# Kernel tuning notes

Hardware: AMD Instinct MI355X
Metric: run time of the kernel (lower is better)

The kernel has to match this reference:

```python
import jax, jax.numpy as jnp
import numpy as np

DIM1, DIM2, NUM_ANS = 1024, 1024, 1000
B, T = 64, 128


def setup_inputs() -> dict:
    key = jax.random.key(0)
    ks = jax.random.split(key, 12)
    H, D_IN = DIM1, DIM1 + DIM2
    s = 0.02
    return {
        "data1": jax.random.normal(ks[0], (B, T, DIM1), dtype=jnp.float32),
        "data2": jax.random.normal(ks[1], (B, T, DIM2), dtype=jnp.float32),
        # layer-1 LSTM (input D_IN -> hidden H), PyTorch gate order i,f,g,o
        "W_ih1": jax.random.normal(ks[2], (4 * H, D_IN), dtype=jnp.float32) * s,
        "W_hh1": jax.random.normal(ks[3], (4 * H, H), dtype=jnp.float32) * s,
        "b1": jax.random.normal(ks[4], (4 * H,), dtype=jnp.float32) * s,
        # layer-2 LSTM (H -> H)
        "W_ih2": jax.random.normal(ks[5], (4 * H, H), dtype=jnp.float32) * s,
        "W_hh2": jax.random.normal(ks[6], (4 * H, H), dtype=jnp.float32) * s,
        "b2": jax.random.normal(ks[7], (4 * H,), dtype=jnp.float32) * s,
        # predict MLP: dim1 -> dim1//4 -> num_ans
        "Wp1": jax.random.normal(ks[8], (DIM1, DIM1 // 4), dtype=jnp.float32) * s,
        "bp1": jnp.zeros((DIM1 // 4,), dtype=jnp.float32),
        "Wp2": jax.random.normal(ks[9], (DIM1 // 4, NUM_ANS), dtype=jnp.float32) * s,
        "bp2": jnp.zeros((NUM_ANS,), dtype=jnp.float32),
    }


def _lstm_cell(x, h, c, Wih, Whh, b):
    gates = x @ Wih.T + h @ Whh.T + b  # [B, 4H]
    i, f, g, o = jnp.split(gates, 4, axis=-1)
    c_new = jax.nn.sigmoid(f) * c + jax.nn.sigmoid(i) * jnp.tanh(g)
    h_new = jax.nn.sigmoid(o) * jnp.tanh(c_new)
    return h_new, c_new


def reference(data1, data2, W_ih1, W_hh1, b1, W_ih2, W_hh2, b2, Wp1, bp1, Wp2, bp2):
    joint = jnp.concatenate((data1, data2), axis=-1)  # [B, T, dim1+dim2]
    Bb = joint.shape[0]
    H = W_hh1.shape[1]
    z = jnp.zeros((Bb, H), dtype=joint.dtype)

    def step(carry, x_t):
        h1, c1, h2, c2 = carry
        h1, c1 = _lstm_cell(x_t, h1, c1, W_ih1, W_hh1, b1)
        h2, c2 = _lstm_cell(h1, h2, c2, W_ih2, W_hh2, b2)
        out_t = h2 + h1  # residual connection between layers
        return (h1, c1, h2, c2), out_t

    xs = jnp.swapaxes(joint, 0, 1)  # [T, B, D]
    _, outs = jax.lax.scan(step, (z, z, z, z), xs)
    lstm_out = jnp.swapaxes(outs, 0, 1)  # [B, T, H]

    hid = jax.nn.relu(lstm_out @ Wp1 + bp1)  # dropout is identity at inference
    logits = hid @ Wp2 + bp2  # [B, T, num_ans]
    return jax.nn.softmax(jnp.squeeze(logits), axis=-1)
```

## Files before the change

kernel.cpp:

```cpp
#include <hip/hip_runtime.h>
#include <math.h>

#define BB   64
#define TT   128
#define HH   1024
#define DIN  2048
#define G4   4096
#define MALL 8192
#define NANS 1000

typedef __attribute__((ext_vector_type(8))) short bf16x8;
typedef __attribute__((ext_vector_type(4))) float f32x4;
typedef __attribute__((ext_vector_type(4))) unsigned int u32x4;

__device__ __forceinline__ float sigmoidf_(float x) { return 1.0f / (1.0f + expf(-x)); }

__device__ __forceinline__ unsigned short f2bf(float f) {
  unsigned u = __float_as_uint(f);
  u = (u + 0x7fff + ((u >> 16) & 1)) >> 16;
  return (unsigned short)u;
}
__device__ __forceinline__ float bf2f(unsigned short h) {
  return __uint_as_float(((unsigned)h) << 16);
}
__device__ __forceinline__ f32x4 mfma16(bf16x8 a, bf16x8 b, f32x4 c) {
  return __builtin_amdgcn_mfma_f32_16x16x32_bf16(a, b, c, 0, 0, 0);
}

__device__ __forceinline__ void stg_b128_sys(unsigned short* p, u32x4 v) {
  asm volatile("global_store_dwordx4 %0, %1, off sc0 sc1" :: "v"(p), "v"(v) : "memory");
}

__global__ __launch_bounds__(256) void concat_cast(
    const float* __restrict__ a, const float* __restrict__ b,
    unsigned short* __restrict__ o, int rshift, long total)
{
  long idx = ((long)blockIdx.x * 256 + threadIdx.x) * 4;
  if (idx >= total) return;
  int row = (int)(idx >> rshift);
  int col = (int)(idx & ((1L << rshift) - 1));
  int half = 1 << (rshift - 1);
  const float* s = (col < half) ? (a + (size_t)row * half + col)
                                : (b + (size_t)row * half + col - half);
  float4 v = *(const float4*)s;
  ushort4 ov;
  ov.x = f2bf(v.x); ov.y = f2bf(v.y); ov.z = f2bf(v.z); ov.w = f2bf(v.w);
  *(ushort4*)(o + idx) = ov;
}

__global__ __launch_bounds__(256) void cast_bf16(
    const float* __restrict__ s, unsigned short* __restrict__ o, long n)
{
  long idx = ((long)blockIdx.x * 256 + threadIdx.x) * 4;
  if (idx >= n) return;
  float4 v = *(const float4*)(s + idx);
  ushort4 ov;
  ov.x = f2bf(v.x); ov.y = f2bf(v.y); ov.z = f2bf(v.z); ov.w = f2bf(v.w);
  *(ushort4*)(o + idx) = ov;
}

__global__ __launch_bounds__(256) void cvt_wp1(
    const float* __restrict__ Wp1, unsigned short* __restrict__ o)
{
  int idx = blockIdx.x * 256 + threadIdx.x;
  int n = idx >> 10, k = idx & 1023;
  o[idx] = f2bf(Wp1[(size_t)k * 256 + n]);
}

__global__ __launch_bounds__(256) void cvt_wp2(
    const float* __restrict__ Wp2, unsigned short* __restrict__ o)
{
  int idx = blockIdx.x * 256 + threadIdx.x;
  int n = idx >> 8, k = idx & 255;
  o[idx] = f2bf(n < NANS ? Wp2[(size_t)k * NANS + n] : 0.f);
}

__global__ __launch_bounds__(256) void zero_ring(
    float4* __restrict__ a, float4* __restrict__ b, unsigned int* __restrict__ bar)
{
  int i = blockIdx.x * 256 + threadIdx.x;
  if (i < 8192) a[i] = make_float4(0.f, 0.f, 0.f, 0.f);
  else          b[i - 8192] = make_float4(0.f, 0.f, 0.f, 0.f);
  if (i == 0) *bar = 0u;
}

template<int OUT_BF16, int RELU, int PERM>
__global__ __launch_bounds__(256) void mfma_gemm(
    const unsigned short* __restrict__ A,
    const unsigned short* __restrict__ W,
    const float* __restrict__ bias,
    void* __restrict__ Cout,
    int M, int N, int K, int ldc, int nvalid)
{
  __shared__ __align__(16) unsigned short As[128 * 72];
  __shared__ __align__(16) unsigned short Bs[128 * 72];
  const int t = threadIdx.x;
  const int n0 = blockIdx.x * 128, m0 = blockIdx.y * 128;
  const int w = t >> 6, lane = t & 63, lr = lane & 15, q = lane >> 4;
  const int wn = (w & 1) * 64, wm = (w >> 1) * 64;
  f32x4 acc[4][4] = {};
  for (int k0 = 0; k0 < K; k0 += 64) {
    #pragma unroll
    for (int s = 0; s < 4; s++) {
      int ci = s * 256 + t;
      int row = ci >> 3, c = ci & 7;
      bf16x8 va = *(const bf16x8*)(A + (size_t)(m0 + row) * K + k0 + c * 8);
      *(bf16x8*)(As + row * 72 + c * 8) = va;
      bf16x8 vb = *(const bf16x8*)(W + (size_t)(n0 + row) * K + k0 + c * 8);
      *(bf16x8*)(Bs + row * 72 + c * 8) = vb;
    }
    __syncthreads();
    #pragma unroll
    for (int kk = 0; kk < 2; kk++) {
      bf16x8 a[4], b[4];
      #pragma unroll
      for (int mt = 0; mt < 4; mt++)
        a[mt] = *(const bf16x8*)(As + (wm + mt * 16 + lr) * 72 + kk * 32 + q * 8);
      #pragma unroll
      for (int nt = 0; nt < 4; nt++)
        b[nt] = *(const bf16x8*)(Bs + (wn + nt * 16 + lr) * 72 + kk * 32 + q * 8);
      #pragma unroll
      for (int mt = 0; mt < 4; mt++)
        #pragma unroll
        for (int nt = 0; nt < 4; nt++)
          acc[mt][nt] = mfma16(a[mt], b[nt], acc[mt][nt]);
    }
    __syncthreads();
  }
  #pragma unroll
  for (int mt = 0; mt < 4; mt++)
    #pragma unroll
    for (int nt = 0; nt < 4; nt++)
      #pragma unroll
      for (int r = 0; r < 4; r++) {
        int row = m0 + wm + mt * 16 + q * 4 + r;
        int col = n0 + wn + nt * 16 + lr;
        if (col < nvalid) {
          float v = acc[mt][nt][r] + bias[col];
          if (RELU) v = fmaxf(v, 0.f);
          if (PERM) row = ((row & 127) << 6) | (row >> 7);
          if (OUT_BF16)
            ((unsigned short*)Cout)[(size_t)row * ldc + col] = f2bf(v);
          else
            ((float*)Cout)[(size_t)row * ldc + col] = v;
        }
      }
}

__global__ __launch_bounds__(512) void lstm_persist(
    const unsigned short* __restrict__ Whh1b,
    const unsigned short* __restrict__ W2cat,
    const unsigned short* __restrict__ gxb,
    const float* __restrict__ b2,
    unsigned short* __restrict__ hr1,
    unsigned short* __restrict__ hr2,
    unsigned short* __restrict__ lob,
    unsigned int* __restrict__ bar)
{
  __shared__ float red[4][64][34];
  __shared__ __align__(16) unsigned short hst[64][8];
  const int t = threadIdx.x;
  const int w = t >> 6, lane = t & 63, lr = lane & 15, q = lane >> 4;
  const int kq = w & 3, rh = w >> 2;
  const bool isA = (blockIdx.x < 128);
  const int j0 = (isA ? blockIdx.x : blockIdx.x - 128) * 8;
  const int g0 = lr >> 2, u0 = lr & 3;
  const int cm = t >> 3, cu = t & 7, ju = j0 + cu;
  const int cb = (cu >> 2) * 17 + (cu & 3);
  float creg = 0.f;

  const unsigned short* wpA0 =
      Whh1b + (size_t)(g0 * 1024 + j0 + u0) * 1024 + kq * 256 + q * 8;
  const unsigned short* wpA1 = wpA0 + 4 * 1024;
  const unsigned short* wpB0 =
      W2cat + (size_t)(g0 * 1024 + j0 + u0) * 2048 + kq * 512 + q * 8;
  const unsigned short* wpB1 = wpB0 + 4 * 2048;

  for (int p = 0; p <= TT; p++) {
    if (isA) {
      if (p < TT) {
        const unsigned short* h1p = hr1 + (size_t)p * 65536;
        const unsigned short* gp = gxb + ((size_t)(p << 6) + cm) * 4096 + ju;
        unsigned short gi = gp[0], gf = gp[1024], gg2 = gp[2048], go = gp[3072];
        {
          const int kof = kq * 256 + q * 8;
          const unsigned short* hb = h1p + (size_t)(rh * 32 + lr) * 1024 + kof;
          f32x4 acc[2][2] = {};
          #pragma unroll
          for (int ks = 0; ks < 8; ks++) {
            bf16x8 b0 = *(const bf16x8*)(wpA0 + ks * 32);
            bf16x8 b1 = *(const bf16x8*)(wpA1 + ks * 32);
            #pragma unroll
            for (int mt = 0; mt < 2; mt++) {
              bf16x8 af = *(const bf16x8*)(hb + (size_t)(mt * 16) * 1024 + ks * 32);
              acc[mt][0] = mfma16(af, b0, acc[mt][0]);
              acc[mt][1] = mfma16(af, b1, acc[mt][1]);
            }
          }
          #pragma unroll
          for (int mt = 0; mt < 2; mt++)
            #pragma unroll
            for (int r = 0; r < 4; r++) {
              red[kq][rh * 32 + mt * 16 + q * 4 + r][lr]      = acc[mt][0][r];
              red[kq][rh * 32 + mt * 16 + q * 4 + r][17 + lr] = acc[mt][1][r];
            }
        }
        __syncthreads();
        float s[4];
        #pragma unroll
        for (int gg = 0; gg < 4; gg++)
          s[gg] = red[0][cm][cb + gg * 4] + red[1][cm][cb + gg * 4]
                + red[2][cm][cb + gg * 4] + red[3][cm][cb + gg * 4];
        s[0] += bf2f(gi); s[1] += bf2f(gf); s[2] += bf2f(gg2); s[3] += bf2f(go);
        float i_ = sigmoidf_(s[0]), f_ = sigmoidf_(s[1]);
        float g_ = tanhf(s[2]), o_ = sigmoidf_(s[3]);
        float c = f_ * creg + i_ * g_;
        creg = c;
        hst[cm][cu] = f2bf(o_ * tanhf(c));
        __syncthreads();
        if (t < 64) {
          u32x4 v = *(const u32x4*)(&hst[t][0]);
          stg_b128_sys(hr1 + (size_t)(p + 1) * 65536 + t * 1024 + j0, v);
        }
        asm volatile("s_waitcnt vmcnt(0)" ::: "memory");
      }
    } else {
      if (p > 0) {
        const unsigned short* h1p = hr1 + (size_t)p * 65536;
        const unsigned short* h2p = hr2 + (size_t)(p - 1) * 65536;
        {
          const int kof = kq * 512 + q * 8;
          const unsigned short* hb = (kq < 2)
              ? (h1p + (size_t)(rh * 32 + lr) * 1024 + kof)
              : (h2p + (size_t)(rh * 32 + lr) * 1024 + (kof - 1024));
          f32x4 acc[2][2] = {};
          #pragma unroll
          for (int ks = 0; ks < 16; ks++) {
            bf16x8 b0 = *(const bf16x8*)(wpB0 + ks * 32);
            bf16x8 b1 = *(const bf16x8*)(wpB1 + ks * 32);
            #pragma unroll
            for (int mt = 0; mt < 2; mt++) {
              bf16x8 af = *(const bf16x8*)(hb + (size_t)(mt * 16) * 1024 + ks * 32);
              acc[mt][0] = mfma16(af, b0, acc[mt][0]);
              acc[mt][1] = mfma16(af, b1, acc[mt][1]);
            }
          }
          #pragma unroll
          for (int mt = 0; mt < 2; mt++)
            #pragma unroll
            for (int r = 0; r < 4; r++) {
              red[kq][rh * 32 + mt * 16 + q * 4 + r][lr]      = acc[mt][0][r];
              red[kq][rh * 32 + mt * 16 + q * 4 + r][17 + lr] = acc[mt][1][r];
            }
        }
        __syncthreads();
        float s[4];
        #pragma unroll
        for (int gg = 0; gg < 4; gg++)
          s[gg] = red[0][cm][cb + gg * 4] + red[1][cm][cb + gg * 4]
                + red[2][cm][cb + gg * 4] + red[3][cm][cb + gg * 4]
                + b2[gg * 1024 + ju];
        float i_ = sigmoidf_(s[0]), f_ = sigmoidf_(s[1]);
        float g_ = tanhf(s[2]), o_ = sigmoidf_(s[3]);
        float c = f_ * creg + i_ * g_;
        creg = c;
        float h2v = o_ * tanhf(c);
        hst[cm][cu] = f2bf(h2v);
        float h1v = bf2f(h1p[(size_t)cm * 1024 + ju]);
        lob[((size_t)(cm << 7) + (p - 1)) * 1024 + ju] = f2bf(h1v + h2v);
        __syncthreads();
        if (t < 64) {
          u32x4 v = *(const u32x4*)(&hst[t][0]);
          stg_b128_sys(hr2 + (size_t)p * 65536 + t * 1024 + j0, v);
        }
        asm volatile("s_waitcnt vmcnt(0)" ::: "memory");
      }
    }

    if (p < TT) {
      __syncthreads();
      if (t == 0) {
        __hip_atomic_fetch_add(bar, 1u, __ATOMIC_RELAXED, __HIP_MEMORY_SCOPE_AGENT);
        const unsigned tgt = 256u * (unsigned)(p + 1);
        unsigned iters = 0;
        while (__hip_atomic_load(bar, __ATOMIC_RELAXED, __HIP_MEMORY_SCOPE_AGENT) < tgt) {
          __builtin_amdgcn_s_sleep(1);
          if (++iters > 100000000u) break;
        }
      }
      __syncthreads();
    }
  }
}

__global__ __launch_bounds__(256) void softmax_k(float* __restrict__ out)
{
  __shared__ float smax[4];
  __shared__ float ssum[4];
  const int m = blockIdx.x;
  const int t = threadIdx.x;
  const int lane = t & 63, wid = t >> 6;
  const bool act = (t < 250);
  float x[4] = {0.f, 0.f, 0.f, 0.f};
  if (act) *(float4*)x = *(const float4*)(out + (size_t)m * NANS + t * 4);
  float v = act ? fmaxf(fmaxf(x[0], x[1]), fmaxf(x[2], x[3])) : -1e30f;
  #pragma unroll
  for (int o = 32; o > 0; o >>= 1) v = fmaxf(v, __shfl_down(v, o));
  if (lane == 0) smax[wid] = v;
  __syncthreads();
  const float mx = fmaxf(fmaxf(smax[0], smax[1]), fmaxf(smax[2], smax[3]));
  float e[4] = {0.f, 0.f, 0.f, 0.f};
  float s = 0.f;
  if (act) {
    e[0] = expf(x[0] - mx); e[1] = expf(x[1] - mx);
    e[2] = expf(x[2] - mx); e[3] = expf(x[3] - mx);
    s = (e[0] + e[1]) + (e[2] + e[3]);
  }
  #pragma unroll
  for (int o = 32; o > 0; o >>= 1) s += __shfl_down(s, o);
  if (lane == 0) ssum[wid] = s;
  __syncthreads();
  const float inv = 1.0f / (((ssum[0] + ssum[1]) + (ssum[2] + ssum[3])));
  if (act) {
    float4 o4 = make_float4(e[0] * inv, e[1] * inv, e[2] * inv, e[3] * inv);
    *(float4*)(out + (size_t)m * NANS + t * 4) = o4;
  }
}

extern "C" void kernel_launch(void* const* d_in, const int* in_sizes, int n_in,
                              void* d_out, int out_size, void* d_ws, size_t ws_size,
                              hipStream_t stream)
{
  const float* d1   = (const float*)d_in[0];
  const float* d2   = (const float*)d_in[1];
  const float* Wih1 = (const float*)d_in[2];
  const float* Whh1 = (const float*)d_in[3];
  const float* b1   = (const float*)d_in[4];
  const float* Wih2 = (const float*)d_in[5];
  const float* Whh2 = (const float*)d_in[6];
  const float* b2   = (const float*)d_in[7];
  const float* Wp1  = (const float*)d_in[8];
  const float* bp1  = (const float*)d_in[9];
  const float* Wp2  = (const float*)d_in[10];
  const float* bp2  = (const float*)d_in[11];
  float* out = (float*)d_out;

  unsigned char* p = (unsigned char*)d_ws;
  unsigned short* gxb   = (unsigned short*)p;  p += 67108864;
  unsigned short* jb    = (unsigned short*)p;  p += 33554432;
  unsigned short* Wb1   = (unsigned short*)p;  p += 16777216;
  unsigned short* W2cat = (unsigned short*)p;  p += 16777216;
  unsigned short* Whh1b = (unsigned short*)p;  p += 8388608;
  unsigned short* lob   = (unsigned short*)p;  p += 16777216;
  unsigned short* hidb  = (unsigned short*)p;  p += 4194304;
  unsigned short* Wp1t  = (unsigned short*)p;  p += 524288;
  unsigned short* Wp2t  = (unsigned short*)p;  p += 524288;
  unsigned int*   bar   = (unsigned int*)p;    p += 256;
  if (ws_size < (size_t)(p - (unsigned char*)d_ws)) return;

  unsigned short* hr1 = jb;
  unsigned short* hr2 = jb + (size_t)129 * 65536;

  concat_cast<<<16384, 256, 0, stream>>>(d1, d2, jb, 11, 16777216L);
  cast_bf16<<<8192, 256, 0, stream>>>(Wih1, Wb1, 8388608L);
  cast_bf16<<<4096, 256, 0, stream>>>(Whh1, Whh1b, 4194304L);
  concat_cast<<<8192, 256, 0, stream>>>(Wih2, Whh2, W2cat, 11, 8388608L);
  cvt_wp1<<<1024, 256, 0, stream>>>(Wp1, Wp1t);
  cvt_wp2<<<1024, 256, 0, stream>>>(Wp2, Wp2t);

  mfma_gemm<1, 0, 1><<<dim3(32, 64), 256, 0, stream>>>(
      jb, Wb1, b1, gxb, MALL, G4, DIN, G4, G4);

  zero_ring<<<64, 256, 0, stream>>>((float4*)hr1, (float4*)hr2, bar);

  lstm_persist<<<256, 512, 0, stream>>>(Whh1b, W2cat, gxb, b2, hr1, hr2, lob, bar);

  mfma_gemm<1, 1, 0><<<dim3(2, 64), 256, 0, stream>>>(
      lob, Wp1t, bp1, hidb, MALL, 256, 1024, 256, 256);
  mfma_gemm<0, 0, 0><<<dim3(8, 64), 256, 0, stream>>>(
      hidb, Wp2t, bp2, out, MALL, 1024, 256, NANS, NANS);
  softmax_k<<<MALL, 256, 0, stream>>>(out);
}
```

Before: 3.181 ms.

## Replace atomic grid barrier with flag-based master barrier and prefetch h via asm loads

Replaces the single atomic-counter grid barrier with per-block arrival flags on separate cache lines. Block 0 gathers all 256 flags and then writes per-block release flags. Each step now issues all hidden-state loads up front through inline-asm global loads into registers, followed by one vmcnt wait, before the MFMA loop. It also adds launch_bounds occupancy of 2. The aim is to cut atomic contention and load-latency serialization in the latency-bound recurrent loop, at the cost of more registers and an extra hop through block 0 for release.

```diff
diff --git a/kernel.cpp b/kernel.cpp
--- a/kernel.cpp
+++ b/kernel.cpp
@@ -30,6 +30,16 @@
 __device__ __forceinline__ void stg_b128_sys(unsigned short* p, u32x4 v) {
   asm volatile("global_store_dwordx4 %0, %1, off sc0 sc1" :: "v"(p), "v"(v) : "memory");
 }
+__device__ __forceinline__ void stg_u32_sys(unsigned int* p, unsigned v) {
+  asm volatile("global_store_dword %0, %1, off sc0 sc1" :: "v"(p), "v"(v) : "memory");
+}
+__device__ __forceinline__ void ldg_b128(bf16x8* d, const unsigned short* p) {
+  asm volatile("global_load_dwordx4 %0, %1, off" : "=v"(*d) : "v"(p));
+}
+#define VMEM_FENCE() do { \
+  asm volatile("s_waitcnt vmcnt(0)" ::: "memory"); \
+  __builtin_amdgcn_sched_barrier(0); \
+} while (0)
 
 __global__ __launch_bounds__(256) void concat_cast(
     const float* __restrict__ a, const float* __restrict__ b,
@@ -76,12 +86,13 @@
 }
 
 __global__ __launch_bounds__(256) void zero_ring(
-    float4* __restrict__ a, float4* __restrict__ b, unsigned int* __restrict__ bar)
+    float4* __restrict__ a, float4* __restrict__ b, float4* __restrict__ f)
 {
   int i = blockIdx.x * 256 + threadIdx.x;
-  if (i < 8192) a[i] = make_float4(0.f, 0.f, 0.f, 0.f);
-  else          b[i - 8192] = make_float4(0.f, 0.f, 0.f, 0.f);
-  if (i == 0) *bar = 0u;
+  float4 z = make_float4(0.f, 0.f, 0.f, 0.f);
+  if (i < 8192)       a[i] = z;
+  else if (i < 16384) b[i - 8192] = z;
+  else if (i < 18432) f[i - 16384] = z;
 }
 
 template<int OUT_BF16, int RELU, int PERM>
@@ -147,7 +158,7 @@
       }
 }
 
-__global__ __launch_bounds__(512) void lstm_persist(
+__global__ __launch_bounds__(512, 2) void lstm_persist(
     const unsigned short* __restrict__ Whh1b,
     const unsigned short* __restrict__ W2cat,
     const unsigned short* __restrict__ gxb,
@@ -155,7 +166,8 @@
     unsigned short* __restrict__ hr1,
     unsigned short* __restrict__ hr2,
     unsigned short* __restrict__ lob,
-    unsigned int* __restrict__ bar)
+    unsigned int* __restrict__ abar,
+    unsigned int* __restrict__ rbar)
 {
   __shared__ float red[4][64][34];
   __shared__ __align__(16) unsigned short hst[64][8];
@@ -182,20 +194,27 @@
         const unsigned short* h1p = hr1 + (size_t)p * 65536;
         const unsigned short* gp = gxb + ((size_t)(p << 6) + cm) * 4096 + ju;
         unsigned short gi = gp[0], gf = gp[1024], gg2 = gp[2048], go = gp[3072];
+        bf16x8 hreg[16];
         {
           const int kof = kq * 256 + q * 8;
           const unsigned short* hb = h1p + (size_t)(rh * 32 + lr) * 1024 + kof;
+          #pragma unroll
+          for (int ks = 0; ks < 8; ks++) {
+            ldg_b128(&hreg[2 * ks],     hb + ks * 32);
+            ldg_b128(&hreg[2 * ks + 1], hb + (size_t)16 * 1024 + ks * 32);
+          }
+        }
+        VMEM_FENCE();
+        {
           f32x4 acc[2][2] = {};
           #pragma unroll
           for (int ks = 0; ks < 8; ks++) {
             bf16x8 b0 = *(const bf16x8*)(wpA0 + ks * 32);
             bf16x8 b1 = *(const bf16x8*)(wpA1 + ks * 32);
-            #pragma unroll
-            for (int mt = 0; mt < 2; mt++) {
-              bf16x8 af = *(const bf16x8*)(hb + (size_t)(mt * 16) * 1024 + ks * 32);
-              acc[mt][0] = mfma16(af, b0, acc[mt][0]);
-              acc[mt][1] = mfma16(af, b1, acc[mt][1]);
-            }
+            acc[0][0] = mfma16(hreg[2 * ks],     b0, acc[0][0]);
+            acc[0][1] = mfma16(hreg[2 * ks],     b1, acc[0][1]);
+            acc[1][0] = mfma16(hreg[2 * ks + 1], b0, acc[1][0]);
+            acc[1][1] = mfma16(hreg[2 * ks + 1], b1, acc[1][1]);
           }
           #pragma unroll
           for (int mt = 0; mt < 2; mt++)
@@ -228,22 +247,29 @@
       if (p > 0) {
         const unsigned short* h1p = hr1 + (size_t)p * 65536;
         const unsigned short* h2p = hr2 + (size_t)(p - 1) * 65536;
+        bf16x8 hreg[32];
         {
           const int kof = kq * 512 + q * 8;
           const unsigned short* hb = (kq < 2)
               ? (h1p + (size_t)(rh * 32 + lr) * 1024 + kof)
               : (h2p + (size_t)(rh * 32 + lr) * 1024 + (kof - 1024));
+          #pragma unroll
+          for (int ks = 0; ks < 16; ks++) {
+            ldg_b128(&hreg[2 * ks],     hb + ks * 32);
+            ldg_b128(&hreg[2 * ks + 1], hb + (size_t)16 * 1024 + ks * 32);
+          }
+        }
+        VMEM_FENCE();
+        {
           f32x4 acc[2][2] = {};
           #pragma unroll
           for (int ks = 0; ks < 16; ks++) {
             bf16x8 b0 = *(const bf16x8*)(wpB0 + ks * 32);
             bf16x8 b1 = *(const bf16x8*)(wpB1 + ks * 32);
-            #pragma unroll
-            for (int mt = 0; mt < 2; mt++) {
-              bf16x8 af = *(const bf16x8*)(hb + (size_t)(mt * 16) * 1024 + ks * 32);
-              acc[mt][0] = mfma16(af, b0, acc[mt][0]);
-              acc[mt][1] = mfma16(af, b1, acc[mt][1]);
-            }
+            acc[0][0] = mfma16(hreg[2 * ks],     b0, acc[0][0]);
+            acc[0][1] = mfma16(hreg[2 * ks],     b1, acc[0][1]);
+            acc[1][0] = mfma16(hreg[2 * ks + 1], b0, acc[1][0]);
+            acc[1][1] = mfma16(hreg[2 * ks + 1], b1, acc[1][1]);
           }
           #pragma unroll
           for (int mt = 0; mt < 2; mt++)
@@ -279,12 +305,27 @@
 
     if (p < TT) {
       __syncthreads();
+      const unsigned tgt = (unsigned)(p + 1);
+      if (t == 0)
+        stg_u32_sys(abar + (size_t)blockIdx.x * 16, tgt);
+      if (blockIdx.x == 0) {
+        if (t < 256) {
+          const unsigned int* fp = abar + (size_t)t * 16;
+          unsigned iters = 0;
+          while (__hip_atomic_load(fp, __ATOMIC_RELAXED, __HIP_MEMORY_SCOPE_AGENT) < tgt) {
+            __builtin_amdgcn_s_sleep(2);
+            if (++iters > 100000000u) break;
+          }
+        }
+        __syncthreads();
+        if (t < 256)
+          stg_u32_sys(rbar + (size_t)t * 16, tgt);
+      }
       if (t == 0) {
-        __hip_atomic_fetch_add(bar, 1u, __ATOMIC_RELAXED, __HIP_MEMORY_SCOPE_AGENT);
-        const unsigned tgt = 256u * (unsigned)(p + 1);
+        const unsigned int* rp = rbar + (size_t)blockIdx.x * 16;
         unsigned iters = 0;
-        while (__hip_atomic_load(bar, __ATOMIC_RELAXED, __HIP_MEMORY_SCOPE_AGENT) < tgt) {
-          __builtin_amdgcn_s_sleep(1);
+        while (__hip_atomic_load(rp, __ATOMIC_RELAXED, __HIP_MEMORY_SCOPE_AGENT) < tgt) {
+          __builtin_amdgcn_s_sleep(2);
           if (++iters > 100000000u) break;
         }
       }
@@ -355,7 +396,8 @@
   unsigned short* hidb  = (unsigned short*)p;  p += 4194304;
   unsigned short* Wp1t  = (unsigned short*)p;  p += 524288;
   unsigned short* Wp2t  = (unsigned short*)p;  p += 524288;
-  unsigned int*   bar   = (unsigned int*)p;    p += 256;
+  unsigned int*   abar  = (unsigned int*)p;    p += 16384;
+  unsigned int*   rbar  = (unsigned int*)p;    p += 16384;
   if (ws_size < (size_t)(p - (unsigned char*)d_ws)) return;
 
   unsigned short* hr1 = jb;
@@ -371,9 +413,10 @@
   mfma_gemm<1, 0, 1><<<dim3(32, 64), 256, 0, stream>>>(
       jb, Wb1, b1, gxb, MALL, G4, DIN, G4, G4);
 
-  zero_ring<<<64, 256, 0, stream>>>((float4*)hr1, (float4*)hr2, bar);
-
-  lstm_persist<<<256, 512, 0, stream>>>(Whh1b, W2cat, gxb, b2, hr1, hr2, lob, bar);
+  zero_ring<<<72, 256, 0, stream>>>((float4*)hr1, (float4*)hr2, (float4*)abar);
+
+  lstm_persist<<<256, 512, 0, stream>>>(Whh1b, W2cat, gxb, b2, hr1, hr2, lob,
+                                        abar, rbar);
 
   mfma_gemm<1, 1, 0><<<dim3(2, 64), 256, 0, stream>>>(
       lob, Wp1t, bp1, hidb, MALL, 256, 1024, 256, 256);
```

New measurement: 2.610 ms. -17.9%, faster.
